# Optimization experiments

Hardware: AMD Instinct MI355X
Metric: run time of the kernel (lower is better)

## Reference

```python
import jax, jax.numpy as jnp
import numpy as np

N, T, H, KQ, V = 8, 256, 8, 128, 32  # batch, seq (Tq=Tk=T), heads, kq_dim, value_dim(=latent_dim)
SCALE = 1.0 / np.sqrt(KQ)


def setup_inputs() -> dict:
    k = jax.random.split(jax.random.key(0), 10)
    w = 0.05
    return {
        "value": jax.random.normal(k[0], (N, T, V), dtype=jnp.float32),
        "key": jax.random.normal(k[1], (N, T, KQ), dtype=jnp.float32),
        "query": jax.random.normal(k[2], (N, T, KQ), dtype=jnp.float32),
        "mask": jax.random.randint(k[3], (N, T, V), 0, 2, dtype=jnp.int32),
        # attn_linear[0]: query proj, attn_linear[1]: key proj (torch Linear: y = x @ W.T + b)
        "Wq": jax.random.normal(k[4], (H * KQ, KQ), dtype=jnp.float32) * w,
        "bq": jax.random.normal(k[5], (H * KQ,), dtype=jnp.float32) * w,
        "Wk": jax.random.normal(k[6], (H * KQ, KQ), dtype=jnp.float32) * w,
        "bk": jax.random.normal(k[7], (H * KQ,), dtype=jnp.float32) * w,
        "Wo": jax.random.normal(k[8], (V, H * V), dtype=jnp.float32) * w,  # attn_out: Linear(ld*H, ld), ld == V
        "bo": jax.random.normal(k[9], (V,), dtype=jnp.float32) * w,
    }


def reference(value, key, query, mask, Wq, bq, Wk, bk, Wo, bo):
    n, t, vdim = value.shape
    nq, tq, _ = query.shape
    nk, tk, _ = key.shape
    h = Wq.shape[0] // query.shape[-1]
    kq = query.shape[-1]

    # per-head projections: (N, H, T, KQ)
    hq = (query @ Wq.T + bq).reshape(nq, tq, h, kq).transpose(0, 2, 1, 3)
    hk = (key @ Wk.T + bk).reshape(nk, tk, h, kq).transpose(0, 2, 1, 3)

    # scores: (N, H, Tq, Tk), then broadcast per value-dim -> (N, H, Tq, Tk, V)
    scores = jnp.einsum("nhqd,nhkd->nhqk", hq, hk) * jnp.asarray(SCALE, value.dtype)
    scores = jnp.broadcast_to(scores[..., None], (n, h, tq, tk, vdim))

    # mask (N, Tk, V): mask[i,t,d]==0 means value[i,t,d] unobserved
    m = mask[:, None, None, :, :]  # (N,1,1,Tk,V)
    scores = jnp.where(m == 0, jnp.asarray(-1e9, scores.dtype), scores)

    p_attn = jax.nn.softmax(scores, axis=-2)  # softmax over Tk, per value-dim

    # weighted sum over keys: (N, H, Tq, V) -> (N, Tq, H*V)
    out = jnp.einsum("nhqkv,nkv->nqhv", p_attn, value).reshape(n, tq, h * vdim)
    out_rep = out @ Wo.T + bo  # (N, Tq, ld)
    return out_rep, p_attn
```

## Files before the change

kernel.cpp:

```cpp
#include <hip/hip_runtime.h>

#define N_ 8
#define T_ 256
#define H_ 8
#define KQ_ 128
#define V_ 32

typedef float f32x4 __attribute__((ext_vector_type(4)));

__global__ __launch_bounds__(256) void proj_kernel(
    const float* __restrict__ query, const float* __restrict__ key,
    const float* __restrict__ Wq, const float* __restrict__ bq,
    const float* __restrict__ Wk, const float* __restrict__ bk,
    float* __restrict__ hqT, float* __restrict__ hkT)
{
  int b = blockIdx.x;
  int dh = b & 1;
  int h  = (b >> 1) & 7;
  int n  = (b >> 4) & 7;
  int proj = (b >> 7) & 1;
  const float* src  = proj ? key : query;
  const float* W    = proj ? Wk  : Wq;
  const float* bias = proj ? bk  : bq;
  float* dst        = proj ? hkT : hqT;
  int d0 = dh * 64;

  __shared__ float qs[256 * 36];
  __shared__ float ws[64 * 36];

  int tl   = threadIdx.x & 31;
  int dsub = threadIdx.x >> 5;
  const float* qsrc = src + (size_t)n * T_ * KQ_;
  const float* wsrc = W + (size_t)(h * KQ_ + d0) * KQ_;

  float acc[8][8];
#pragma unroll
  for (int it = 0; it < 8; ++it)
#pragma unroll
    for (int dd = 0; dd < 8; ++dd) acc[it][dd] = 0.f;

  for (int kc = 0; kc < 4; ++kc) {
    if (kc) __syncthreads();
    {
      int r = threadIdx.x >> 3, c4 = (threadIdx.x & 7) * 4;
#pragma unroll
      for (int rep = 0; rep < 8; ++rep) {
        int row = r + rep * 32;
        *(float4*)&qs[row * 36 + c4] =
            *(const float4*)&qsrc[(size_t)row * KQ_ + kc * 32 + c4];
      }
#pragma unroll
      for (int rep = 0; rep < 2; ++rep) {
        int row = r + rep * 32;
        *(float4*)&ws[row * 36 + c4] =
            *(const float4*)&wsrc[(size_t)row * KQ_ + kc * 32 + c4];
      }
    }
    __syncthreads();

#pragma unroll 2
    for (int j0 = 0; j0 < 32; j0 += 4) {
      float4 qv[8];
#pragma unroll
      for (int it = 0; it < 8; ++it)
        qv[it] = *(const float4*)&qs[(tl + 32 * it) * 36 + j0];
#pragma unroll
      for (int dd = 0; dd < 8; ++dd) {
        float4 w4 = *(const float4*)&ws[(dsub * 8 + dd) * 36 + j0];
#pragma unroll
        for (int it = 0; it < 8; ++it) {
          acc[it][dd] = fmaf(qv[it].x, w4.x, acc[it][dd]);
          acc[it][dd] = fmaf(qv[it].y, w4.y, acc[it][dd]);
          acc[it][dd] = fmaf(qv[it].z, w4.z, acc[it][dd]);
          acc[it][dd] = fmaf(qv[it].w, w4.w, acc[it][dd]);
        }
      }
    }
  }

#pragma unroll
  for (int dd = 0; dd < 8; ++dd) {
    int d = d0 + dsub * 8 + dd;
    float bb = bias[h * KQ_ + d];
    size_t base = (((size_t)n * H_ + h) * KQ_ + d) * T_;
#pragma unroll
    for (int it = 0; it < 8; ++it)
      dst[base + it * 32 + tl] = acc[it][dd] + bb;
  }
}

__global__ __launch_bounds__(64) void attn_kernel(
    const float* __restrict__ hqT, const float* __restrict__ hkT,
    const int* __restrict__ mask, const float* __restrict__ value,
    float* __restrict__ p_out, float* __restrict__ out_ws)
{
  const float SCALE = 0.08838834764831845f;
  int b = blockIdx.x;
  int q0 = (b & 31) * 8;
  int h  = (b >> 5) & 7;
  int n  = b >> 8;
  int l  = threadIdx.x;
  int row0 = (n * H_ + h) * T_ + q0;

  __shared__ float hq_s[KQ_ * 12];
  __shared__ float e_s[T_ * 8];
  __shared__ float inv_s[8 * 32];

  const float* hqbase = hqT + ((size_t)n * H_ + h) * KQ_ * T_;
  const float* hkbase = hkT + ((size_t)n * H_ + h) * KQ_ * T_;

#pragma unroll
  for (int rep = 0; rep < 16; ++rep) {
    int i = l + 64 * rep;
    int j = i >> 3, qq = i & 7;
    hq_s[j * 12 + qq] = hqbase[(size_t)j * T_ + q0 + qq];
  }
  __syncthreads();

  float acc[4][8];
#pragma unroll
  for (int i = 0; i < 4; ++i)
#pragma unroll
    for (int qq = 0; qq < 8; ++qq) acc[i][qq] = 0.f;

#pragma unroll 4
  for (int j = 0; j < KQ_; ++j) {
    float hk0 = hkbase[(size_t)j * T_ + l];
    float hk1 = hkbase[(size_t)j * T_ + l + 64];
    float hk2 = hkbase[(size_t)j * T_ + l + 128];
    float hk3 = hkbase[(size_t)j * T_ + l + 192];
    float4 a0 = *(const float4*)&hq_s[j * 12];
    float4 a1 = *(const float4*)&hq_s[j * 12 + 4];
    acc[0][0] = fmaf(a0.x, hk0, acc[0][0]); acc[0][1] = fmaf(a0.y, hk0, acc[0][1]);
    acc[0][2] = fmaf(a0.z, hk0, acc[0][2]); acc[0][3] = fmaf(a0.w, hk0, acc[0][3]);
    acc[0][4] = fmaf(a1.x, hk0, acc[0][4]); acc[0][5] = fmaf(a1.y, hk0, acc[0][5]);
    acc[0][6] = fmaf(a1.z, hk0, acc[0][6]); acc[0][7] = fmaf(a1.w, hk0, acc[0][7]);
    acc[1][0] = fmaf(a0.x, hk1, acc[1][0]); acc[1][1] = fmaf(a0.y, hk1, acc[1][1]);
    acc[1][2] = fmaf(a0.z, hk1, acc[1][2]); acc[1][3] = fmaf(a0.w, hk1, acc[1][3]);
    acc[1][4] = fmaf(a1.x, hk1, acc[1][4]); acc[1][5] = fmaf(a1.y, hk1, acc[1][5]);
    acc[1][6] = fmaf(a1.z, hk1, acc[1][6]); acc[1][7] = fmaf(a1.w, hk1, acc[1][7]);
    acc[2][0] = fmaf(a0.x, hk2, acc[2][0]); acc[2][1] = fmaf(a0.y, hk2, acc[2][1]);
    acc[2][2] = fmaf(a0.z, hk2, acc[2][2]); acc[2][3] = fmaf(a0.w, hk2, acc[2][3]);
    acc[2][4] = fmaf(a1.x, hk2, acc[2][4]); acc[2][5] = fmaf(a1.y, hk2, acc[2][5]);
    acc[2][6] = fmaf(a1.z, hk2, acc[2][6]); acc[2][7] = fmaf(a1.w, hk2, acc[2][7]);
    acc[3][0] = fmaf(a0.x, hk3, acc[3][0]); acc[3][1] = fmaf(a0.y, hk3, acc[3][1]);
    acc[3][2] = fmaf(a0.z, hk3, acc[3][2]); acc[3][3] = fmaf(a0.w, hk3, acc[3][3]);
    acc[3][4] = fmaf(a1.x, hk3, acc[3][4]); acc[3][5] = fmaf(a1.y, hk3, acc[3][5]);
    acc[3][6] = fmaf(a1.z, hk3, acc[3][6]); acc[3][7] = fmaf(a1.w, hk3, acc[3][7]);
  }

  {
#pragma unroll
    for (int qq = 0; qq < 8; ++qq) {
      float m = fmaxf(fmaxf(acc[0][qq] * SCALE, acc[1][qq] * SCALE),
                      fmaxf(acc[2][qq] * SCALE, acc[3][qq] * SCALE));
      for (int off = 32; off >= 1; off >>= 1)
        m = fmaxf(m, __shfl_xor(m, off, 64));
#pragma unroll
      for (int i = 0; i < 4; ++i)
        acc[i][qq] = __expf(acc[i][qq] * SCALE - m);
    }
  }
#pragma unroll
  for (int i = 0; i < 4; ++i) {
    int k = l + 64 * i;
    *(f32x4*)&e_s[k * 8]     = f32x4{acc[i][0], acc[i][1], acc[i][2], acc[i][3]};
    *(f32x4*)&e_s[k * 8 + 4] = f32x4{acc[i][4], acc[i][5], acc[i][6], acc[i][7]};
  }
  __syncthreads();

  const int*   mrow = mask  + (size_t)n * T_ * V_;
  const float* vrow = value + (size_t)n * T_ * V_;
  int v = l & 31, kh = l >> 5;
  float s8[8], o8[8];
#pragma unroll
  for (int qq = 0; qq < 8; ++qq) { s8[qq] = 0.f; o8[qq] = 0.f; }
#pragma unroll 4
  for (int i = 0; i < 128; ++i) {
    int k = kh * 128 + i;
    float mf = (float)mrow[k * V_ + v];
    float vv = vrow[k * V_ + v];
    float4 e0 = *(const float4*)&e_s[k * 8];
    float4 e1 = *(const float4*)&e_s[k * 8 + 4];
    float p;
    p = e0.x * mf; s8[0] += p; o8[0] = fmaf(p, vv, o8[0]);
    p = e0.y * mf; s8[1] += p; o8[1] = fmaf(p, vv, o8[1]);
    p = e0.z * mf; s8[2] += p; o8[2] = fmaf(p, vv, o8[2]);
    p = e0.w * mf; s8[3] += p; o8[3] = fmaf(p, vv, o8[3]);
    p = e1.x * mf; s8[4] += p; o8[4] = fmaf(p, vv, o8[4]);
    p = e1.y * mf; s8[5] += p; o8[5] = fmaf(p, vv, o8[5]);
    p = e1.z * mf; s8[6] += p; o8[6] = fmaf(p, vv, o8[6]);
    p = e1.w * mf; s8[7] += p; o8[7] = fmaf(p, vv, o8[7]);
  }
#pragma unroll
  for (int qq = 0; qq < 8; ++qq) {
    s8[qq] += __shfl_xor(s8[qq], 32, 64);
    o8[qq] += __shfl_xor(o8[qq], 32, 64);
  }
  if (kh == 0) {
#pragma unroll
    for (int qq = 0; qq < 8; ++qq) {
      float inv = 1.0f / s8[qq];
      inv_s[qq * 32 + v] = inv;
      out_ws[(((size_t)n * T_ + q0 + qq) * H_ + h) * V_ + v] = o8[qq] * inv;
    }
  }
  __syncthreads();

  {
    int v0 = (l & 7) * 4;
    f32x4 iv[8];
#pragma unroll
    for (int qq = 0; qq < 8; ++qq)
      iv[qq] = *(const f32x4*)&inv_s[qq * 32 + v0];
    f32x4* pbase = (f32x4*)p_out + (size_t)row0 * 2048;

#pragma unroll 4
    for (int rep = 0; rep < 32; ++rep) {
      int e4 = rep * 64 + l;
      int k  = rep * 8 + (l >> 3);
      const int4 m4 = *(const int4*)&mrow[k * V_ + v0];
      float fx = (float)m4.x, fy = (float)m4.y, fz = (float)m4.z, fw = (float)m4.w;
      f32x4 e0 = *(const f32x4*)&e_s[k * 8];
      f32x4 e1 = *(const f32x4*)&e_s[k * 8 + 4];
      float e[8] = {e0.x, e0.y, e0.z, e0.w, e1.x, e1.y, e1.z, e1.w};
#pragma unroll
      for (int qq = 0; qq < 8; ++qq) {
        f32x4 pv;
        pv.x = e[qq] * fx * iv[qq].x;
        pv.y = e[qq] * fy * iv[qq].y;
        pv.z = e[qq] * fz * iv[qq].z;
        pv.w = e[qq] * fw * iv[qq].w;
        __builtin_nontemporal_store(pv, &pbase[(size_t)qq * 2048 + e4]);
      }
    }
  }
}

__global__ __launch_bounds__(256) void outproj_kernel(
    const float* __restrict__ out_ws, const float* __restrict__ Wo,
    const float* __restrict__ bo, float* __restrict__ out_rep)
{
  __shared__ float wot[256 * 33];
  __shared__ float rows_s[4 * 256];
  __shared__ float red[4 * 32];
  int r0 = blockIdx.x * 4;
  for (int i = threadIdx.x; i < 32 * 256; i += 256) {
    int o = i >> 8, c = i & 255;
    wot[c * 33 + o] = Wo[i];
  }
  for (int i = threadIdx.x; i < 4 * 256; i += 256)
    rows_s[i] = out_ws[(size_t)r0 * 256 + i];
  __syncthreads();
  int o  = threadIdx.x & 31;
  int rr = (threadIdx.x >> 5) & 3;
  int kh = threadIdx.x >> 7;
  int cb = kh * 128;
  float acc = 0.f;
#pragma unroll 4
  for (int c = 0; c < 128; ++c)
    acc = fmaf(rows_s[rr * 256 + cb + c], wot[(cb + c) * 33 + o], acc);
  if (kh == 1) red[rr * 32 + o] = acc;
  __syncthreads();
  if (kh == 0)
    out_rep[(size_t)(r0 + rr) * 32 + o] = acc + red[rr * 32 + o] + bo[o];
}

extern "C" void kernel_launch(void* const* d_in, const int* in_sizes, int n_in,
                              void* d_out, int out_size, void* d_ws, size_t ws_size,
                              hipStream_t stream) {
  const float* value = (const float*)d_in[0];
  const float* key   = (const float*)d_in[1];
  const float* query = (const float*)d_in[2];
  const int*   mask  = (const int*)d_in[3];
  const float* Wq = (const float*)d_in[4];
  const float* bq = (const float*)d_in[5];
  const float* Wk = (const float*)d_in[6];
  const float* bk = (const float*)d_in[7];
  const float* Wo = (const float*)d_in[8];
  const float* bo = (const float*)d_in[9];

  float* out_rep = (float*)d_out;
  float* p_out   = (float*)d_out + (size_t)N_ * T_ * V_;

  float* hqT    = (float*)d_ws;
  float* hkT    = hqT + (size_t)N_ * H_ * KQ_ * T_;
  float* out_ws = hkT + (size_t)N_ * H_ * KQ_ * T_;

  hipLaunchKernelGGL(proj_kernel, dim3(256), dim3(256), 0, stream,
                     query, key, Wq, bq, Wk, bk, hqT, hkT);
  hipLaunchKernelGGL(attn_kernel, dim3(2048), dim3(64), 0, stream,
                     hqT, hkT, mask, value, p_out, out_ws);
  hipLaunchKernelGGL(outproj_kernel, dim3(512), dim3(256), 0, stream,
                     out_ws, Wo, bo, out_rep);
}
```

Before: 157.9 us.

## Shrink attention tile to two queries per block and quadruple grid size

```diff
diff --git a/kernel.cpp b/kernel.cpp
--- a/kernel.cpp
+++ b/kernel.cpp
@@ -7,6 +7,7 @@
 #define V_ 32
 
 typedef float f32x4 __attribute__((ext_vector_type(4)));
+typedef float f32x2 __attribute__((ext_vector_type(2)));
 
 __global__ __launch_bounds__(256) void proj_kernel(
     const float* __restrict__ query, const float* __restrict__ key,
@@ -96,123 +97,90 @@
 {
   const float SCALE = 0.08838834764831845f;
   int b = blockIdx.x;
-  int q0 = (b & 31) * 8;
-  int h  = (b >> 5) & 7;
-  int n  = b >> 8;
+  int q0 = (b & 127) * 2;
+  int h  = (b >> 7) & 7;
+  int n  = b >> 10;
   int l  = threadIdx.x;
   int row0 = (n * H_ + h) * T_ + q0;
 
-  __shared__ float hq_s[KQ_ * 12];
-  __shared__ float e_s[T_ * 8];
-  __shared__ float inv_s[8 * 32];
+  __shared__ float hq_s[KQ_ * 2];
+  __shared__ float e_s[T_ * 2];
+  __shared__ float inv_s[2 * 32];
 
   const float* hqbase = hqT + ((size_t)n * H_ + h) * KQ_ * T_;
   const float* hkbase = hkT + ((size_t)n * H_ + h) * KQ_ * T_;
 
 #pragma unroll
-  for (int rep = 0; rep < 16; ++rep) {
+  for (int rep = 0; rep < 4; ++rep) {
     int i = l + 64 * rep;
-    int j = i >> 3, qq = i & 7;
-    hq_s[j * 12 + qq] = hqbase[(size_t)j * T_ + q0 + qq];
-  }
-  __syncthreads();
-
-  float acc[4][8];
-#pragma unroll
-  for (int i = 0; i < 4; ++i)
-#pragma unroll
-    for (int qq = 0; qq < 8; ++qq) acc[i][qq] = 0.f;
+    hq_s[i] = hqbase[(size_t)(i >> 1) * T_ + q0 + (i & 1)];
+  }
+  __syncthreads();
+
+  float acc[4][2];
+#pragma unroll
+  for (int i = 0; i < 4; ++i) { acc[i][0] = 0.f; acc[i][1] = 0.f; }
 
 #pragma unroll 4
   for (int j = 0; j < KQ_; ++j) {
-    float hk0 = hkbase[(size_t)j * T_ + l];
-    float hk1 = hkbase[(size_t)j * T_ + l + 64];
-    float hk2 = hkbase[(size_t)j * T_ + l + 128];
-    float hk3 = hkbase[(size_t)j * T_ + l + 192];
-    float4 a0 = *(const float4*)&hq_s[j * 12];
-    float4 a1 = *(const float4*)&hq_s[j * 12 + 4];
-    acc[0][0] = fmaf(a0.x, hk0, acc[0][0]); acc[0][1] = fmaf(a0.y, hk0, acc[0][1]);
-    acc[0][2] = fmaf(a0.z, hk0, acc[0][2]); acc[0][3] = fmaf(a0.w, hk0, acc[0][3]);
-    acc[0][4] = fmaf(a1.x, hk0, acc[0][4]); acc[0][5] = fmaf(a1.y, hk0, acc[0][5]);
-    acc[0][6] = fmaf(a1.z, hk0, acc[0][6]); acc[0][7] = fmaf(a1.w, hk0, acc[0][7]);
-    acc[1][0] = fmaf(a0.x, hk1, acc[1][0]); acc[1][1] = fmaf(a0.y, hk1, acc[1][1]);
-    acc[1][2] = fmaf(a0.z, hk1, acc[1][2]); acc[1][3] = fmaf(a0.w, hk1, acc[1][3]);
-    acc[1][4] = fmaf(a1.x, hk1, acc[1][4]); acc[1][5] = fmaf(a1.y, hk1, acc[1][5]);
-    acc[1][6] = fmaf(a1.z, hk1, acc[1][6]); acc[1][7] = fmaf(a1.w, hk1, acc[1][7]);
-    acc[2][0] = fmaf(a0.x, hk2, acc[2][0]); acc[2][1] = fmaf(a0.y, hk2, acc[2][1]);
-    acc[2][2] = fmaf(a0.z, hk2, acc[2][2]); acc[2][3] = fmaf(a0.w, hk2, acc[2][3]);
-    acc[2][4] = fmaf(a1.x, hk2, acc[2][4]); acc[2][5] = fmaf(a1.y, hk2, acc[2][5]);
-    acc[2][6] = fmaf(a1.z, hk2, acc[2][6]); acc[2][7] = fmaf(a1.w, hk2, acc[2][7]);
-    acc[3][0] = fmaf(a0.x, hk3, acc[3][0]); acc[3][1] = fmaf(a0.y, hk3, acc[3][1]);
-    acc[3][2] = fmaf(a0.z, hk3, acc[3][2]); acc[3][3] = fmaf(a0.w, hk3, acc[3][3]);
-    acc[3][4] = fmaf(a1.x, hk3, acc[3][4]); acc[3][5] = fmaf(a1.y, hk3, acc[3][5]);
-    acc[3][6] = fmaf(a1.z, hk3, acc[3][6]); acc[3][7] = fmaf(a1.w, hk3, acc[3][7]);
-  }
-
-  {
-#pragma unroll
-    for (int qq = 0; qq < 8; ++qq) {
-      float m = fmaxf(fmaxf(acc[0][qq] * SCALE, acc[1][qq] * SCALE),
-                      fmaxf(acc[2][qq] * SCALE, acc[3][qq] * SCALE));
-      for (int off = 32; off >= 1; off >>= 1)
-        m = fmaxf(m, __shfl_xor(m, off, 64));
-#pragma unroll
-      for (int i = 0; i < 4; ++i)
-        acc[i][qq] = __expf(acc[i][qq] * SCALE - m);
-    }
+    float4 hk = *(const float4*)&hkbase[(size_t)j * T_ + 4 * l];
+    f32x2 a = *(const f32x2*)&hq_s[j * 2];
+    acc[0][0] = fmaf(a.x, hk.x, acc[0][0]); acc[0][1] = fmaf(a.y, hk.x, acc[0][1]);
+    acc[1][0] = fmaf(a.x, hk.y, acc[1][0]); acc[1][1] = fmaf(a.y, hk.y, acc[1][1]);
+    acc[2][0] = fmaf(a.x, hk.z, acc[2][0]); acc[2][1] = fmaf(a.y, hk.z, acc[2][1]);
+    acc[3][0] = fmaf(a.x, hk.w, acc[3][0]); acc[3][1] = fmaf(a.y, hk.w, acc[3][1]);
+  }
+
+#pragma unroll
+  for (int qq = 0; qq < 2; ++qq) {
+    float m = fmaxf(fmaxf(acc[0][qq], acc[1][qq]),
+                    fmaxf(acc[2][qq], acc[3][qq])) * SCALE;
+    for (int off = 32; off >= 1; off >>= 1)
+      m = fmaxf(m, __shfl_xor(m, off, 64));
+#pragma unroll
+    for (int i = 0; i < 4; ++i)
+      acc[i][qq] = __expf(acc[i][qq] * SCALE - m);
   }
 #pragma unroll
   for (int i = 0; i < 4; ++i) {
-    int k = l + 64 * i;
-    *(f32x4*)&e_s[k * 8]     = f32x4{acc[i][0], acc[i][1], acc[i][2], acc[i][3]};
-    *(f32x4*)&e_s[k * 8 + 4] = f32x4{acc[i][4], acc[i][5], acc[i][6], acc[i][7]};
+    int k = 4 * l + i;
+    *(f32x2*)&e_s[k * 2] = f32x2{acc[i][0], acc[i][1]};
   }
   __syncthreads();
 
   const int*   mrow = mask  + (size_t)n * T_ * V_;
   const float* vrow = value + (size_t)n * T_ * V_;
   int v = l & 31, kh = l >> 5;
-  float s8[8], o8[8];
-#pragma unroll
-  for (int qq = 0; qq < 8; ++qq) { s8[qq] = 0.f; o8[qq] = 0.f; }
+  float s2[2] = {0.f, 0.f}, o2[2] = {0.f, 0.f};
 #pragma unroll 4
   for (int i = 0; i < 128; ++i) {
     int k = kh * 128 + i;
     float mf = (float)mrow[k * V_ + v];
     float vv = vrow[k * V_ + v];
-    float4 e0 = *(const float4*)&e_s[k * 8];
-    float4 e1 = *(const float4*)&e_s[k * 8 + 4];
+    f32x2 e = *(const f32x2*)&e_s[k * 2];
     float p;
-    p = e0.x * mf; s8[0] += p; o8[0] = fmaf(p, vv, o8[0]);
-    p = e0.y * mf; s8[1] += p; o8[1] = fmaf(p, vv, o8[1]);
-    p = e0.z * mf; s8[2] += p; o8[2] = fmaf(p, vv, o8[2]);
-    p = e0.w * mf; s8[3] += p; o8[3] = fmaf(p, vv, o8[3]);
-    p = e1.x * mf; s8[4] += p; o8[4] = fmaf(p, vv, o8[4]);
-    p = e1.y * mf; s8[5] += p; o8[5] = fmaf(p, vv, o8[5]);
-    p = e1.z * mf; s8[6] += p; o8[6] = fmaf(p, vv, o8[6]);
-    p = e1.w * mf; s8[7] += p; o8[7] = fmaf(p, vv, o8[7]);
-  }
-#pragma unroll
-  for (int qq = 0; qq < 8; ++qq) {
-    s8[qq] += __shfl_xor(s8[qq], 32, 64);
-    o8[qq] += __shfl_xor(o8[qq], 32, 64);
+    p = e.x * mf; s2[0] += p; o2[0] = fmaf(p, vv, o2[0]);
+    p = e.y * mf; s2[1] += p; o2[1] = fmaf(p, vv, o2[1]);
+  }
+#pragma unroll
+  for (int qq = 0; qq < 2; ++qq) {
+    s2[qq] += __shfl_xor(s2[qq], 32, 64);
+    o2[qq] += __shfl_xor(o2[qq], 32, 64);
   }
   if (kh == 0) {
 #pragma unroll
-    for (int qq = 0; qq < 8; ++qq) {
-      float inv = 1.0f / s8[qq];
+    for (int qq = 0; qq < 2; ++qq) {
+      float inv = 1.0f / s2[qq];
       inv_s[qq * 32 + v] = inv;
-      out_ws[(((size_t)n * T_ + q0 + qq) * H_ + h) * V_ + v] = o8[qq] * inv;
+      out_ws[(((size_t)n * T_ + q0 + qq) * H_ + h) * V_ + v] = o2[qq] * inv;
     }
   }
   __syncthreads();
 
   {
     int v0 = (l & 7) * 4;
-    f32x4 iv[8];
-#pragma unroll
-    for (int qq = 0; qq < 8; ++qq)
-      iv[qq] = *(const f32x4*)&inv_s[qq * 32 + v0];
+    f32x4 iv0 = *(const f32x4*)&inv_s[v0];
+    f32x4 iv1 = *(const f32x4*)&inv_s[32 + v0];
     f32x4* pbase = (f32x4*)p_out + (size_t)row0 * 2048;
 
 #pragma unroll 4
@@ -221,18 +189,14 @@
       int k  = rep * 8 + (l >> 3);
       const int4 m4 = *(const int4*)&mrow[k * V_ + v0];
       float fx = (float)m4.x, fy = (float)m4.y, fz = (float)m4.z, fw = (float)m4.w;
-      f32x4 e0 = *(const f32x4*)&e_s[k * 8];
-      f32x4 e1 = *(const f32x4*)&e_s[k * 8 + 4];
-      float e[8] = {e0.x, e0.y, e0.z, e0.w, e1.x, e1.y, e1.z, e1.w};
-#pragma unroll
-      for (int qq = 0; qq < 8; ++qq) {
-        f32x4 pv;
-        pv.x = e[qq] * fx * iv[qq].x;
-        pv.y = e[qq] * fy * iv[qq].y;
-        pv.z = e[qq] * fz * iv[qq].z;
-        pv.w = e[qq] * fw * iv[qq].w;
-        __builtin_nontemporal_store(pv, &pbase[(size_t)qq * 2048 + e4]);
-      }
+      f32x2 e = *(const f32x2*)&e_s[k * 2];
+      f32x4 pv0, pv1;
+      pv0.x = e.x * fx * iv0.x; pv0.y = e.x * fy * iv0.y;
+      pv0.z = e.x * fz * iv0.z; pv0.w = e.x * fw * iv0.w;
+      pv1.x = e.y * fx * iv1.x; pv1.y = e.y * fy * iv1.y;
+      pv1.z = e.y * fz * iv1.z; pv1.w = e.y * fw * iv1.w;
+      __builtin_nontemporal_store(pv0, &pbase[e4]);
+      __builtin_nontemporal_store(pv1, &pbase[2048 + e4]);
     }
   }
 }
@@ -289,7 +253,7 @@
 
   hipLaunchKernelGGL(proj_kernel, dim3(256), dim3(256), 0, stream,
                      query, key, Wq, bq, Wk, bk, hqT, hkT);
-  hipLaunchKernelGGL(attn_kernel, dim3(2048), dim3(64), 0, stream,
+  hipLaunchKernelGGL(attn_kernel, dim3(8192), dim3(64), 0, stream,
                      hqT, hkT, mask, value, p_out, out_ws);
   hipLaunchKernelGGL(outproj_kernel, dim3(512), dim3(256), 0, stream,
                      out_ws, Wo, bo, out_rep);
```

After: 163.3 us. 3.4% more time.

## Split attention block work across two wavefronts with cross-wave softmax reduction

Applied to the files above, without the earlier changes.

```diff
diff --git a/kernel.cpp b/kernel.cpp
--- a/kernel.cpp
+++ b/kernel.cpp
@@ -89,7 +89,7 @@
   }
 }
 
-__global__ __launch_bounds__(64) void attn_kernel(
+__global__ __launch_bounds__(128) void attn_kernel(
     const float* __restrict__ hqT, const float* __restrict__ hkT,
     const int* __restrict__ mask, const float* __restrict__ value,
     float* __restrict__ p_out, float* __restrict__ out_ws)
@@ -99,36 +99,38 @@
   int q0 = (b & 31) * 8;
   int h  = (b >> 5) & 7;
   int n  = b >> 8;
-  int l  = threadIdx.x;
+  int t  = threadIdx.x;
+  int w  = t >> 6;
   int row0 = (n * H_ + h) * T_ + q0;
 
   __shared__ float hq_s[KQ_ * 12];
   __shared__ float e_s[T_ * 8];
   __shared__ float inv_s[8 * 32];
+  __shared__ float wred[2 * 8];
+  __shared__ float red_s[8 * 32];
+  __shared__ float red_o[8 * 32];
 
   const float* hqbase = hqT + ((size_t)n * H_ + h) * KQ_ * T_;
   const float* hkbase = hkT + ((size_t)n * H_ + h) * KQ_ * T_;
 
 #pragma unroll
-  for (int rep = 0; rep < 16; ++rep) {
-    int i = l + 64 * rep;
+  for (int rep = 0; rep < 8; ++rep) {
+    int i = t + 128 * rep;
     int j = i >> 3, qq = i & 7;
     hq_s[j * 12 + qq] = hqbase[(size_t)j * T_ + q0 + qq];
   }
   __syncthreads();
 
-  float acc[4][8];
-#pragma unroll
-  for (int i = 0; i < 4; ++i)
+  float acc[2][8];
+#pragma unroll
+  for (int i = 0; i < 2; ++i)
 #pragma unroll
     for (int qq = 0; qq < 8; ++qq) acc[i][qq] = 0.f;
 
 #pragma unroll 4
   for (int j = 0; j < KQ_; ++j) {
-    float hk0 = hkbase[(size_t)j * T_ + l];
-    float hk1 = hkbase[(size_t)j * T_ + l + 64];
-    float hk2 = hkbase[(size_t)j * T_ + l + 128];
-    float hk3 = hkbase[(size_t)j * T_ + l + 192];
+    float hk0 = hkbase[(size_t)j * T_ + t];
+    float hk1 = hkbase[(size_t)j * T_ + t + 128];
     float4 a0 = *(const float4*)&hq_s[j * 12];
     float4 a1 = *(const float4*)&hq_s[j * 12 + 4];
     acc[0][0] = fmaf(a0.x, hk0, acc[0][0]); acc[0][1] = fmaf(a0.y, hk0, acc[0][1]);
@@ -139,45 +141,44 @@
     acc[1][2] = fmaf(a0.z, hk1, acc[1][2]); acc[1][3] = fmaf(a0.w, hk1, acc[1][3]);
     acc[1][4] = fmaf(a1.x, hk1, acc[1][4]); acc[1][5] = fmaf(a1.y, hk1, acc[1][5]);
     acc[1][6] = fmaf(a1.z, hk1, acc[1][6]); acc[1][7] = fmaf(a1.w, hk1, acc[1][7]);
-    acc[2][0] = fmaf(a0.x, hk2, acc[2][0]); acc[2][1] = fmaf(a0.y, hk2, acc[2][1]);
-    acc[2][2] = fmaf(a0.z, hk2, acc[2][2]); acc[2][3] = fmaf(a0.w, hk2, acc[2][3]);
-    acc[2][4] = fmaf(a1.x, hk2, acc[2][4]); acc[2][5] = fmaf(a1.y, hk2, acc[2][5]);
-    acc[2][6] = fmaf(a1.z, hk2, acc[2][6]); acc[2][7] = fmaf(a1.w, hk2, acc[2][7]);
-    acc[3][0] = fmaf(a0.x, hk3, acc[3][0]); acc[3][1] = fmaf(a0.y, hk3, acc[3][1]);
-    acc[3][2] = fmaf(a0.z, hk3, acc[3][2]); acc[3][3] = fmaf(a0.w, hk3, acc[3][3]);
-    acc[3][4] = fmaf(a1.x, hk3, acc[3][4]); acc[3][5] = fmaf(a1.y, hk3, acc[3][5]);
-    acc[3][6] = fmaf(a1.z, hk3, acc[3][6]); acc[3][7] = fmaf(a1.w, hk3, acc[3][7]);
-  }
-
+  }
+
+  float mloc[8];
+#pragma unroll
+  for (int qq = 0; qq < 8; ++qq) {
+    float m = fmaxf(acc[0][qq], acc[1][qq]) * SCALE;
+    for (int off = 32; off >= 1; off >>= 1)
+      m = fmaxf(m, __shfl_xor(m, off, 64));
+    mloc[qq] = m;
+  }
+  if ((t & 63) == 0) {
+#pragma unroll
+    for (int qq = 0; qq < 8; ++qq) wred[w * 8 + qq] = mloc[qq];
+  }
+  __syncthreads();
   {
 #pragma unroll
     for (int qq = 0; qq < 8; ++qq) {
-      float m = fmaxf(fmaxf(acc[0][qq] * SCALE, acc[1][qq] * SCALE),
-                      fmaxf(acc[2][qq] * SCALE, acc[3][qq] * SCALE));
-      for (int off = 32; off >= 1; off >>= 1)
-        m = fmaxf(m, __shfl_xor(m, off, 64));
-#pragma unroll
-      for (int i = 0; i < 4; ++i)
-        acc[i][qq] = __expf(acc[i][qq] * SCALE - m);
-    }
-  }
-#pragma unroll
-  for (int i = 0; i < 4; ++i) {
-    int k = l + 64 * i;
-    *(f32x4*)&e_s[k * 8]     = f32x4{acc[i][0], acc[i][1], acc[i][2], acc[i][3]};
-    *(f32x4*)&e_s[k * 8 + 4] = f32x4{acc[i][4], acc[i][5], acc[i][6], acc[i][7]};
+      float mx = fmaxf(wred[qq], wred[8 + qq]);
+      acc[0][qq] = __expf(acc[0][qq] * SCALE - mx);
+      acc[1][qq] = __expf(acc[1][qq] * SCALE - mx);
+    }
+    *(f32x4*)&e_s[t * 8]           = f32x4{acc[0][0], acc[0][1], acc[0][2], acc[0][3]};
+    *(f32x4*)&e_s[t * 8 + 4]       = f32x4{acc[0][4], acc[0][5], acc[0][6], acc[0][7]};
+    *(f32x4*)&e_s[(t + 128) * 8]     = f32x4{acc[1][0], acc[1][1], acc[1][2], acc[1][3]};
+    *(f32x4*)&e_s[(t + 128) * 8 + 4] = f32x4{acc[1][4], acc[1][5], acc[1][6], acc[1][7]};
   }
   __syncthreads();
 
   const int*   mrow = mask  + (size_t)n * T_ * V_;
   const float* vrow = value + (size_t)n * T_ * V_;
-  int v = l & 31, kh = l >> 5;
+  int v = t & 31, kg = t >> 5;
   float s8[8], o8[8];
 #pragma unroll
   for (int qq = 0; qq < 8; ++qq) { s8[qq] = 0.f; o8[qq] = 0.f; }
 #pragma unroll 4
-  for (int i = 0; i < 128; ++i) {
-    int k = kh * 128 + i;
+  for (int i = 0; i < 64; ++i) {
+    int k = kg * 64 + i;
     float mf = (float)mrow[k * V_ + v];
     float vv = vrow[k * V_ + v];
     float4 e0 = *(const float4*)&e_s[k * 8];
@@ -197,18 +198,28 @@
     s8[qq] += __shfl_xor(s8[qq], 32, 64);
     o8[qq] += __shfl_xor(o8[qq], 32, 64);
   }
-  if (kh == 0) {
+  if (w == 1 && (t & 63) < 32) {
 #pragma unroll
     for (int qq = 0; qq < 8; ++qq) {
-      float inv = 1.0f / s8[qq];
+      red_s[qq * 32 + v] = s8[qq];
+      red_o[qq * 32 + v] = o8[qq];
+    }
+  }
+  __syncthreads();
+  if (w == 0 && (t & 63) < 32) {
+#pragma unroll
+    for (int qq = 0; qq < 8; ++qq) {
+      float s = s8[qq] + red_s[qq * 32 + v];
+      float o = o8[qq] + red_o[qq * 32 + v];
+      float inv = 1.0f / s;
       inv_s[qq * 32 + v] = inv;
-      out_ws[(((size_t)n * T_ + q0 + qq) * H_ + h) * V_ + v] = o8[qq] * inv;
+      out_ws[(((size_t)n * T_ + q0 + qq) * H_ + h) * V_ + v] = o * inv;
     }
   }
   __syncthreads();
 
   {
-    int v0 = (l & 7) * 4;
+    int v0 = (t & 7) * 4;
     f32x4 iv[8];
 #pragma unroll
     for (int qq = 0; qq < 8; ++qq)
@@ -216,9 +227,9 @@
     f32x4* pbase = (f32x4*)p_out + (size_t)row0 * 2048;
 
 #pragma unroll 4
-    for (int rep = 0; rep < 32; ++rep) {
-      int e4 = rep * 64 + l;
-      int k  = rep * 8 + (l >> 3);
+    for (int rep = 0; rep < 16; ++rep) {
+      int e4 = rep * 128 + t;
+      int k  = rep * 16 + (t >> 3);
       const int4 m4 = *(const int4*)&mrow[k * V_ + v0];
       float fx = (float)m4.x, fy = (float)m4.y, fz = (float)m4.z, fw = (float)m4.w;
       f32x4 e0 = *(const f32x4*)&e_s[k * 8];
@@ -289,7 +300,7 @@
 
   hipLaunchKernelGGL(proj_kernel, dim3(256), dim3(256), 0, stream,
                      query, key, Wq, bq, Wk, bk, hqT, hkT);
-  hipLaunchKernelGGL(attn_kernel, dim3(2048), dim3(64), 0, stream,
+  hipLaunchKernelGGL(attn_kernel, dim3(2048), dim3(128), 0, stream,
                      hqT, hkT, mask, value, p_out, out_ws);
   hipLaunchKernelGGL(outproj_kernel, dim3(512), dim3(256), 0, stream,
                      out_ws, Wo, bo, out_rep);
```

New measurement: 158.6 us. About the same (+0.4%).
